# Kernel optimization log

Hardware: AMD Instinct MI355X
Metric: run time of the kernel (lower is better)

The kernel has to match this reference:

```python
import jax, jax.numpy as jnp
import numpy as np

N_NODES = 100000
N_EDGES = 1600000
D_IN = 128
D_OUT = 128


def setup_inputs() -> dict:
    key = jax.random.key(0)
    ks = jax.random.split(key, 7)
    x = jax.random.normal(ks[0], (N_NODES, D_IN), dtype=jnp.float32)
    edge_index = jax.random.randint(ks[1], (2, N_EDGES), 0, N_NODES, dtype=jnp.int64)
    edge_weights = jax.random.uniform(ks[2], (N_EDGES,), dtype=jnp.float32)
    s = 1.0 / np.sqrt(D_IN)
    W_lin = jax.random.uniform(ks[3], (D_IN, D_OUT), minval=-s, maxval=s, dtype=jnp.float32)
    b_lin = jax.random.uniform(ks[4], (D_OUT,), minval=-s, maxval=s, dtype=jnp.float32)
    W_agg = jax.random.uniform(ks[5], (D_IN, D_OUT), minval=-s, maxval=s, dtype=jnp.float32)
    b_agg = jax.random.uniform(ks[6], (D_OUT,), minval=-s, maxval=s, dtype=jnp.float32)
    return {"x": x, "edge_index": edge_index, "edge_weights": edge_weights,
            "W_lin": W_lin, "b_lin": b_lin, "W_agg": W_agg, "b_agg": b_agg}


def reference(x, edge_index, edge_weights, W_lin, b_lin, W_agg, b_agg):
    # self transform: [N, D_out]
    self_features = x @ W_lin + b_lin
    row, col = edge_index[0], edge_index[1]
    # gather neighbor features along edges: [E, D_in]
    neighbor_features = x[col] * edge_weights[:, None]
    # per-edge transform: [E, D_out]
    msgs = neighbor_features @ W_agg + b_agg
    # scatter-add to destination nodes (index_add_ on row)
    aggregated = jax.ops.segment_sum(msgs, row, num_segments=x.shape[0])
    return self_features + aggregated
```

## Files before the change

kernel.cpp:

```cpp
#include <hip/hip_runtime.h>

#define N_NODES 100000
#define N_EDGES 1600000
#define D 128
#define SCAN_CHUNK 1024
#define NB_SCAN ((N_NODES + SCAN_CHUNK - 1) / SCAN_CHUNK)

#define BSHIFT 9
#define BUCK_NODES 512
#define NBUCK 196
#define SCAP 10240
#define PART_CHUNK 4096
#define PART_BLOCKS ((N_EDGES + PART_CHUNK - 1) / PART_CHUNK)
#define CONV_BLOCKS 6250
#define W_BLOCKS 128
#define OCT_DIV 12500

typedef __attribute__((ext_vector_type(8))) short bf16x8;
typedef __attribute__((ext_vector_type(4))) float f32x4;
typedef __attribute__((ext_vector_type(4))) unsigned u32x4;

__device__ __forceinline__ unsigned bf16rne(float f) {
  unsigned u = __float_as_uint(f);
  return (u + 0x7fffu + ((u >> 16) & 1u)) >> 16;
}

#define T5_OFF    200
#define T5_FRAGW  100304
#define T5_SRT    116688
#define T5_XH     3316688
#define T5_ZH     9718736
#define WS_T5_BYTES ((size_t)16120784 * 4)

#define WS_OFF   100000
#define WS_BSUM  200004
#define WS_SRT   200192
#define WS_XH    3400192
#define WS_T1_BYTES ((size_t)3400192 * 4)
#define WS_T2_BYTES ((size_t)(3400192 + 6400000) * 4)

__global__ __launch_bounds__(256) void part_kernel(
    const int* __restrict__ ei, const float* __restrict__ ew,
    const float* __restrict__ x,
    const float* __restrict__ Wl, const float* __restrict__ Wa,
    int* __restrict__ pcur, int2* __restrict__ stage,
    uint4* __restrict__ xh4, unsigned short* __restrict__ fragW) {
  __shared__ int cntL[256];
  __shared__ int s0[256];
  __shared__ int gb[NBUCK];
  __shared__ int curL[NBUCK];
  __shared__ int2 recL[PART_CHUNK];
  __shared__ unsigned char buckL[PART_CHUNK];
  int bid = blockIdx.x, tid = threadIdx.x;

  if (bid < PART_BLOCKS) {
    cntL[tid] = 0;
    __syncthreads();
    int e0 = bid * PART_CHUNK;
    int tot = min(PART_CHUNK, N_EDGES - e0);
#pragma unroll
    for (int k = 0; k < PART_CHUNK / 256; k++) {
      int e = e0 + k * 256 + tid;
      if (e < N_EDGES) atomicAdd(&cntL[ei[e] >> BSHIFT], 1);
    }
    __syncthreads();
    for (int o = 1; o < 256; o <<= 1) {
      int add = (tid >= o) ? s0[tid - o] : 0;
      if (o == 1) add = (tid >= 1) ? cntL[tid - 1] : 0;
      if (o == 1) s0[tid] = cntL[tid];
      __syncthreads();
      if (o > 1) s0[tid] += add;
      else s0[tid] += add - cntL[tid] + cntL[tid];
      __syncthreads();
    }
    s0[tid] = cntL[tid];
    __syncthreads();
    for (int o = 1; o < 256; o <<= 1) {
      int add = (tid >= o) ? s0[tid - o] : 0;
      __syncthreads();
      s0[tid] += add;
      __syncthreads();
    }
    if (tid < NBUCK) {
      gb[tid] = atomicAdd(&pcur[tid], cntL[tid]);
      curL[tid] = 0;
    }
    __syncthreads();
#pragma unroll
    for (int k = 0; k < PART_CHUNK / 256; k++) {
      int e = e0 + k * 256 + tid;
      if (e < N_EDGES) {
        int d = ei[e];
        int src = ei[N_EDGES + e];
        float w = ew[e];
        int b = d >> BSHIFT;
        int r = atomicAdd(&curL[b], 1);
        int slot = (s0[b] - cntL[b]) + r;
        recL[slot] = make_int2(src | ((d & (BUCK_NODES - 1)) << 17),
                               __float_as_int(w));
        buckL[slot] = (unsigned char)b;
      }
    }
    __syncthreads();
    for (int i = tid; i < tot; i += 256) {
      int b = buckL[i];
      int idx = gb[b] + (i - (s0[b] - cntL[b]));
      stage[(size_t)b * SCAP + idx] = recL[i];
    }
  } else if (bid < PART_BLOCKS + CONV_BLOCKS) {
    int g = (bid - PART_BLOCKS) * 256 + tid;
    const u32x4* xp = reinterpret_cast<const u32x4*>(x);
    u32x4 a = __builtin_nontemporal_load(xp + (size_t)g * 2);
    u32x4 b = __builtin_nontemporal_load(xp + (size_t)g * 2 + 1);
    uint4 o;
    o.x = bf16rne(__uint_as_float(a.x)) | (bf16rne(__uint_as_float(a.y)) << 16);
    o.y = bf16rne(__uint_as_float(a.z)) | (bf16rne(__uint_as_float(a.w)) << 16);
    o.z = bf16rne(__uint_as_float(b.x)) | (bf16rne(__uint_as_float(b.y)) << 16);
    o.w = bf16rne(__uint_as_float(b.z)) | (bf16rne(__uint_as_float(b.w)) << 16);
    xh4[g] = o;
  } else {
    int tau = (bid - PART_BLOCKS - CONV_BLOCKS) * 256 + tid;
    int slot = tau >> 3, j = tau & 7;
    int lane = slot & 63, ft = slot >> 6;
    int t = ft & 7, s = ft >> 3;
    int kl = (s & 3) * 32 + (lane >> 4) * 8 + j;
    int n = t * 16 + (lane & 15);
    float v = (s < 4 ? Wl : Wa)[kl * 128 + n];
    fragW[slot * 8 + j] = (unsigned short)bf16rne(v);
  }
}

__global__ __launch_bounds__(512) void binB2_kernel(const int* __restrict__ pcur,
                                                    const int2* __restrict__ stage,
                                                    int* __restrict__ off,
                                                    int2* __restrict__ srt) {
  __shared__ int pc[NBUCK];
  __shared__ int h[BUCK_NODES * 8];
  __shared__ int sa[BUCK_NODES];
  __shared__ int cur8[BUCK_NODES * 8];
  __shared__ int baseS, mS;
  int b = blockIdx.x, tid = threadIdx.x;
  if (tid < NBUCK) pc[tid] = pcur[tid];
  for (int i = tid; i < BUCK_NODES * 8; i += 512) h[i] = 0;
  __syncthreads();
  if (tid == 0) {
    int s = 0;
    for (int i = 0; i < b; i++) s += pc[i];
    baseS = s;
    mS = pc[b];
  }
  __syncthreads();
  int base = baseS, m = mS;
  const int2* sp = stage + (size_t)b * SCAP;
  for (int r = tid; r < m; r += 512) {
    int rx = sp[r].x;
    int lsrc = rx & 0x1FFFF;
    int ldst = ((unsigned)rx) >> 17;
    atomicAdd(&h[(ldst << 3) + lsrc / OCT_DIV], 1);
  }
  __syncthreads();
  int tot = 0;
#pragma unroll
  for (int j = 0; j < 8; j++) tot += h[(tid << 3) + j];
  sa[tid] = tot;
  __syncthreads();
  for (int o = 1; o < BUCK_NODES; o <<= 1) {
    int add = (tid >= o) ? sa[tid - o] : 0;
    __syncthreads();
    sa[tid] += add;
    __syncthreads();
  }
  int nodeExcl = sa[tid] - tot;
  {
    int run = nodeExcl;
#pragma unroll
    for (int j = 0; j < 8; j++) {
      cur8[(tid << 3) + j] = run;
      run += h[(tid << 3) + j];
    }
  }
  int nb = b << BSHIFT;
  int nn = min(BUCK_NODES, N_NODES - nb);
  if (tid < nn) off[nb + tid] = base + nodeExcl;
  if (tid == 0 && b == NBUCK - 1) off[N_NODES] = base + m;
  __syncthreads();
  for (int r = tid; r < m; r += 512) {
    int2 rec = sp[r];
    int lsrc = rec.x & 0x1FFFF;
    int ldst = ((unsigned)rec.x) >> 17;
    int s = atomicAdd(&cur8[(ldst << 3) + lsrc / OCT_DIV], 1);
    srt[base + s] = make_int2(lsrc, rec.y);
  }
}

__global__ __launch_bounds__(256) void gather_zh_kernel(const unsigned* __restrict__ xh,
                                                        const int* __restrict__ off,
                                                        const int2* __restrict__ srt,
                                                        unsigned* __restrict__ zh) {
  int gid = blockIdx.x * 256 + threadIdx.x;
  int n = gid >> 5;
  int lane = gid & 31;
  int beg = off[n], end = off[n + 1];
  float4 acc = make_float4(0.f, 0.f, 0.f, 0.f);
  int e = beg;
  for (; e + 3 < end; e += 4) {
    int2 r0 = srt[e];
    int2 r1 = srt[e + 1];
    int2 r2 = srt[e + 2];
    int2 r3 = srt[e + 3];
    uint2 p0 = *reinterpret_cast<const uint2*>(xh + (size_t)r0.x * 64 + lane * 2);
    uint2 p1 = *reinterpret_cast<const uint2*>(xh + (size_t)r1.x * 64 + lane * 2);
    uint2 p2 = *reinterpret_cast<const uint2*>(xh + (size_t)r2.x * 64 + lane * 2);
    uint2 p3 = *reinterpret_cast<const uint2*>(xh + (size_t)r3.x * 64 + lane * 2);
    float w0 = __int_as_float(r0.y), w1 = __int_as_float(r1.y);
    float w2 = __int_as_float(r2.y), w3 = __int_as_float(r3.y);
    acc.x = fmaf(w0, __uint_as_float(p0.x << 16), acc.x);
    acc.y = fmaf(w0, __uint_as_float(p0.x & 0xffff0000u), acc.y);
    acc.z = fmaf(w0, __uint_as_float(p0.y << 16), acc.z);
    acc.w = fmaf(w0, __uint_as_float(p0.y & 0xffff0000u), acc.w);
    acc.x = fmaf(w1, __uint_as_float(p1.x << 16), acc.x);
    acc.y = fmaf(w1, __uint_as_float(p1.x & 0xffff0000u), acc.y);
    acc.z = fmaf(w1, __uint_as_float(p1.y << 16), acc.z);
    acc.w = fmaf(w1, __uint_as_float(p1.y & 0xffff0000u), acc.w);
    acc.x = fmaf(w2, __uint_as_float(p2.x << 16), acc.x);
    acc.y = fmaf(w2, __uint_as_float(p2.x & 0xffff0000u), acc.y);
    acc.z = fmaf(w2, __uint_as_float(p2.y << 16), acc.z);
    acc.w = fmaf(w2, __uint_as_float(p2.y & 0xffff0000u), acc.w);
    acc.x = fmaf(w3, __uint_as_float(p3.x << 16), acc.x);
    acc.y = fmaf(w3, __uint_as_float(p3.x & 0xffff0000u), acc.y);
    acc.z = fmaf(w3, __uint_as_float(p3.y << 16), acc.z);
    acc.w = fmaf(w3, __uint_as_float(p3.y & 0xffff0000u), acc.w);
  }
  for (; e < end; e++) {
    int2 r0 = srt[e];
    uint2 p0 = *reinterpret_cast<const uint2*>(xh + (size_t)r0.x * 64 + lane * 2);
    float w0 = __int_as_float(r0.y);
    acc.x = fmaf(w0, __uint_as_float(p0.x << 16), acc.x);
    acc.y = fmaf(w0, __uint_as_float(p0.x & 0xffff0000u), acc.y);
    acc.z = fmaf(w0, __uint_as_float(p0.y << 16), acc.z);
    acc.w = fmaf(w0, __uint_as_float(p0.y & 0xffff0000u), acc.w);
  }
  uint2 o;
  o.x = bf16rne(acc.x) | (bf16rne(acc.y) << 16);
  o.y = bf16rne(acc.z) | (bf16rne(acc.w) << 16);
  *reinterpret_cast<uint2*>(zh + (size_t)n * 64 + lane * 2) = o;
}

__global__ __launch_bounds__(256) void mfma_gemm_kernel(
    const short* __restrict__ xh, const short* __restrict__ zh,
    const short* __restrict__ fragW, const int* __restrict__ off,
    const float* __restrict__ bl, const float* __restrict__ ba,
    float* __restrict__ out) {
  int tid = threadIdx.x;
  int wave = tid >> 6, lane = tid & 63;
  int m = lane & 15, q = lane >> 4;
  int R = blockIdx.x * 64 + wave * 16;
  const short* xrow = xh + (size_t)(R + m) * D + q * 8;
  const short* zrow = zh + (size_t)(R + m) * D + q * 8;
  const short* fw = fragW + (size_t)lane * 8;

  f32x4 acc[8];
#pragma unroll
  for (int t = 0; t < 8; t++) acc[t] = (f32x4){0.f, 0.f, 0.f, 0.f};

#pragma unroll
  for (int s = 0; s < 8; s++) {
    bf16x8 a = *reinterpret_cast<const bf16x8*>(s < 4 ? xrow + s * 32
                                                      : zrow + (s - 4) * 32);
#pragma unroll
    for (int t = 0; t < 8; t++) {
      bf16x8 b = *reinterpret_cast<const bf16x8*>(fw + (size_t)((s * 8 + t) * 64) * 8);
      acc[t] = __builtin_amdgcn_mfma_f32_16x16x32_bf16(a, b, acc[t], 0, 0, 0);
    }
  }

  float blv[8], bav[8];
#pragma unroll
  for (int t = 0; t < 8; t++) {
    blv[t] = bl[t * 16 + m];
    bav[t] = ba[t * 16 + m];
  }
#pragma unroll
  for (int r = 0; r < 4; r++) {
    int row = R + q * 4 + r;
    if (row < N_NODES) {
      float dg = (float)(off[row + 1] - off[row]);
#pragma unroll
      for (int t = 0; t < 8; t++)
        __builtin_nontemporal_store(acc[t][r] + blv[t] + dg * bav[t],
                                    out + (size_t)row * D + t * 16 + m);
    }
  }
}


__global__ __launch_bounds__(256) void hist_kernel(const int* __restrict__ ei,
                                                   int* __restrict__ cnt) {
  int e = blockIdx.x * 256 + threadIdx.x;
  if (e < N_EDGES) atomicAdd(&cnt[ei[e]], 1);
}

__global__ __launch_bounds__(256) void block_sum_kernel(const int* __restrict__ cnt,
                                                        int* __restrict__ bsum) {
  int base = blockIdx.x * SCAN_CHUNK;
  int s = 0;
#pragma unroll
  for (int k = 0; k < 4; k++) {
    int i = base + (int)threadIdx.x + k * 256;
    if (i < N_NODES) s += cnt[i];
  }
  __shared__ int red[4];
  for (int o = 32; o > 0; o >>= 1) s += __shfl_down(s, o, 64);
  if ((threadIdx.x & 63) == 0) red[threadIdx.x >> 6] = s;
  __syncthreads();
  if (threadIdx.x == 0) bsum[blockIdx.x] = red[0] + red[1] + red[2] + red[3];
}

__global__ __launch_bounds__(128) void scan_bsum_kernel(int* __restrict__ bsum,
                                                        int* __restrict__ off) {
  __shared__ int sh[128];
  int t = threadIdx.x;
  int v = (t < NB_SCAN) ? bsum[t] : 0;
  sh[t] = v;
  __syncthreads();
  for (int o = 1; o < 128; o <<= 1) {
    int add = (t >= o) ? sh[t - o] : 0;
    __syncthreads();
    sh[t] += add;
    __syncthreads();
  }
  if (t < NB_SCAN) bsum[t] = sh[t] - v;
  if (t == 0) off[N_NODES] = sh[127];
}

__global__ __launch_bounds__(256) void scan_offsets_kernel(const int* __restrict__ cnt,
                                                           const int* __restrict__ bsum,
                                                           int* __restrict__ off) {
  __shared__ int sh[256];
  int t = threadIdx.x;
  int i0 = blockIdx.x * SCAN_CHUNK + t * 4;
  int c[4];
#pragma unroll
  for (int k = 0; k < 4; k++) c[k] = (i0 + k < N_NODES) ? cnt[i0 + k] : 0;
  int ls = c[0] + c[1] + c[2] + c[3];
  sh[t] = ls;
  __syncthreads();
  for (int o = 1; o < 256; o <<= 1) {
    int add = (t >= o) ? sh[t - o] : 0;
    __syncthreads();
    sh[t] += add;
    __syncthreads();
  }
  int run = bsum[blockIdx.x] + sh[t] - ls;
#pragma unroll
  for (int k = 0; k < 4; k++) {
    if (i0 + k < N_NODES) off[i0 + k] = run;
    run += c[k];
  }
}

__global__ __launch_bounds__(256) void fill_kernel(const int* __restrict__ ei,
                                                   const float* __restrict__ ew,
                                                   const int* __restrict__ off,
                                                   int* __restrict__ cur,
                                                   int2* __restrict__ srt) {
  int e = blockIdx.x * 256 + threadIdx.x;
  if (e >= N_EDGES) return;
  int dst = ei[e];
  int p = off[dst] + atomicAdd(&cur[dst], 1);
  srt[p] = make_int2(ei[N_EDGES + e], __float_as_int(ew[e]));
}

__global__ __launch_bounds__(256) void convert_kernel(const float* __restrict__ x,
                                                      uint4* __restrict__ xh) {
  int i = blockIdx.x * 256 + threadIdx.x;
  const float4* xp = reinterpret_cast<const float4*>(x);
  float4 a = xp[(size_t)i * 2];
  float4 b = xp[(size_t)i * 2 + 1];
  uint4 o;
  o.x = bf16rne(a.x) | (bf16rne(a.y) << 16);
  o.y = bf16rne(a.z) | (bf16rne(a.w) << 16);
  o.z = bf16rne(b.x) | (bf16rne(b.y) << 16);
  o.w = bf16rne(b.z) | (bf16rne(b.w) << 16);
  xh[i] = o;
}

__global__ __launch_bounds__(256) void gather_bf16_kernel(const unsigned* __restrict__ xh,
                                                          const int* __restrict__ off,
                                                          const int2* __restrict__ srt,
                                                          float* __restrict__ z,
                                                          float* __restrict__ degf) {
  int gid = blockIdx.x * 256 + threadIdx.x;
  int n = gid >> 5;
  int lane = gid & 31;
  if (n >= N_NODES) return;
  int beg = off[n], end = off[n + 1];
  float4 acc = make_float4(0.f, 0.f, 0.f, 0.f);
  int e = beg;
  for (; e + 1 < end; e += 2) {
    int2 r0 = srt[e];
    int2 r1 = srt[e + 1];
    uint2 p0 = *reinterpret_cast<const uint2*>(xh + (size_t)r0.x * 64 + lane * 2);
    uint2 p1 = *reinterpret_cast<const uint2*>(xh + (size_t)r1.x * 64 + lane * 2);
    float w0 = __int_as_float(r0.y);
    float w1 = __int_as_float(r1.y);
    acc.x = fmaf(w0, __uint_as_float(p0.x << 16), acc.x);
    acc.y = fmaf(w0, __uint_as_float(p0.x & 0xffff0000u), acc.y);
    acc.z = fmaf(w0, __uint_as_float(p0.y << 16), acc.z);
    acc.w = fmaf(w0, __uint_as_float(p0.y & 0xffff0000u), acc.w);
    acc.x = fmaf(w1, __uint_as_float(p1.x << 16), acc.x);
    acc.y = fmaf(w1, __uint_as_float(p1.x & 0xffff0000u), acc.y);
    acc.z = fmaf(w1, __uint_as_float(p1.y << 16), acc.z);
    acc.w = fmaf(w1, __uint_as_float(p1.y & 0xffff0000u), acc.w);
  }
  if (e < end) {
    int2 r0 = srt[e];
    uint2 p0 = *reinterpret_cast<const uint2*>(xh + (size_t)r0.x * 64 + lane * 2);
    float w0 = __int_as_float(r0.y);
    acc.x = fmaf(w0, __uint_as_float(p0.x << 16), acc.x);
    acc.y = fmaf(w0, __uint_as_float(p0.x & 0xffff0000u), acc.y);
    acc.z = fmaf(w0, __uint_as_float(p0.y << 16), acc.z);
    acc.w = fmaf(w0, __uint_as_float(p0.y & 0xffff0000u), acc.w);
  }
  *reinterpret_cast<float4*>(z + (size_t)n * D + (lane << 2)) = acc;
  if (lane == 0) degf[n] = (float)(end - beg);
}

__global__ __launch_bounds__(256) void gather_f32_kernel(const float* __restrict__ x,
                                                         const int* __restrict__ off,
                                                         const int2* __restrict__ srt,
                                                         float* __restrict__ z,
                                                         float* __restrict__ degf) {
  int gid = blockIdx.x * 256 + threadIdx.x;
  int n = gid >> 5;
  int lane = gid & 31;
  if (n >= N_NODES) return;
  int beg = off[n], end = off[n + 1];
  float4 acc = make_float4(0.f, 0.f, 0.f, 0.f);
  for (int e = beg; e < end; e++) {
    int2 r0 = srt[e];
    float4 x0 = *reinterpret_cast<const float4*>(x + (size_t)r0.x * D + (lane << 2));
    float w0 = __int_as_float(r0.y);
    acc.x = fmaf(w0, x0.x, acc.x); acc.y = fmaf(w0, x0.y, acc.y);
    acc.z = fmaf(w0, x0.z, acc.z); acc.w = fmaf(w0, x0.w, acc.w);
  }
  *reinterpret_cast<float4*>(z + (size_t)n * D + (lane << 2)) = acc;
  if (lane == 0) degf[n] = (float)(end - beg);
}

__global__ __launch_bounds__(256) void scatter_kernel(const float* __restrict__ x,
                                                      const int* __restrict__ ei,
                                                      const float* __restrict__ ew,
                                                      float* __restrict__ z,
                                                      float* __restrict__ deg) {
  long long g = (long long)blockIdx.x * 256 + threadIdx.x;
  int e = (int)(g >> 5);
  int lane = (int)(g & 31);
  if (e >= N_EDGES) return;
  int dst = ei[e];
  int src = ei[N_EDGES + e];
  float w = ew[e];
  float4 xv = *reinterpret_cast<const float4*>(x + (size_t)src * D + (lane << 2));
  float* o = z + (size_t)dst * D + (lane << 2);
  atomicAdd(o + 0, w * xv.x);
  atomicAdd(o + 1, w * xv.y);
  atomicAdd(o + 2, w * xv.z);
  atomicAdd(o + 3, w * xv.w);
  if (lane == 0) atomicAdd(deg + dst, 1.0f);
}

__global__ __launch_bounds__(256) void fused_gemm_kernel(const float* __restrict__ x,
                                                         const float* __restrict__ Wl,
                                                         const float* __restrict__ bl,
                                                         const float* __restrict__ Wa,
                                                         const float* __restrict__ ba,
                                                         const float* __restrict__ deg,
                                                         float* __restrict__ out) {
  __shared__ float xs[32 * 16];
  __shared__ float zs[32 * 16];
  __shared__ float wls[16 * 128];
  __shared__ float was[16 * 128];
  const int tid = threadIdx.x;
  const int row0 = blockIdx.x * 32;
  const int c4 = tid & 31;
  const int r0 = tid >> 5;
  float4 acc[4];
#pragma unroll
  for (int i = 0; i < 4; i++) acc[i] = make_float4(0.f, 0.f, 0.f, 0.f);

  for (int k0 = 0; k0 < D; k0 += 16) {
    {
      int t = tid & 127;
      int r = t >> 2;
      int kc = (t & 3) << 2;
      const float* sp = (tid < 128) ? x : out;
      float* dp = (tid < 128) ? xs : zs;
      *reinterpret_cast<float4*>(dp + r * 16 + kc) =
          *reinterpret_cast<const float4*>(sp + (size_t)(row0 + r) * D + k0 + kc);
    }
#pragma unroll
    for (int i = 0; i < 2; i++) {
      int f = tid + i * 256;
      int kk = f >> 5;
      int cc = (f & 31) << 2;
      *reinterpret_cast<float4*>(wls + kk * 128 + cc) =
          *reinterpret_cast<const float4*>(Wl + (size_t)(k0 + kk) * D + cc);
      *reinterpret_cast<float4*>(was + kk * 128 + cc) =
          *reinterpret_cast<const float4*>(Wa + (size_t)(k0 + kk) * D + cc);
    }
    __syncthreads();
#pragma unroll
    for (int kk = 0; kk < 16; kk++) {
      float4 wl = *reinterpret_cast<const float4*>(wls + kk * 128 + (c4 << 2));
      float4 wa = *reinterpret_cast<const float4*>(was + kk * 128 + (c4 << 2));
#pragma unroll
      for (int rr = 0; rr < 4; rr++) {
        int r2 = r0 + rr * 8;
        float xv = xs[r2 * 16 + kk];
        float zv = zs[r2 * 16 + kk];
        acc[rr].x = fmaf(xv, wl.x, fmaf(zv, wa.x, acc[rr].x));
        acc[rr].y = fmaf(xv, wl.y, fmaf(zv, wa.y, acc[rr].y));
        acc[rr].z = fmaf(xv, wl.z, fmaf(zv, wa.z, acc[rr].z));
        acc[rr].w = fmaf(xv, wl.w, fmaf(zv, wa.w, acc[rr].w));
      }
    }
    __syncthreads();
  }

  float4 blv = *reinterpret_cast<const float4*>(bl + (c4 << 2));
  float4 bav = *reinterpret_cast<const float4*>(ba + (c4 << 2));
#pragma unroll
  for (int rr = 0; rr < 4; rr++) {
    int r = row0 + r0 + rr * 8;
    float d = deg[r];
    float4 o;
    o.x = acc[rr].x + blv.x + d * bav.x;
    o.y = acc[rr].y + blv.y + d * bav.y;
    o.z = acc[rr].z + blv.z + d * bav.z;
    o.w = acc[rr].w + blv.w + d * bav.w;
    *reinterpret_cast<float4*>(out + (size_t)r * D + (c4 << 2)) = o;
  }
}

extern "C" void kernel_launch(void* const* d_in, const int* in_sizes, int n_in,
                              void* d_out, int out_size, void* d_ws, size_t ws_size,
                              hipStream_t stream) {
  const float* x  = (const float*)d_in[0];
  const int*   ei = (const int*)d_in[1];
  const float* ew = (const float*)d_in[2];
  const float* Wl = (const float*)d_in[3];
  const float* bl = (const float*)d_in[4];
  const float* Wa = (const float*)d_in[5];
  const float* ba = (const float*)d_in[6];
  float* out = (float*)d_out;

  if (ws_size >= WS_T5_BYTES) {
    int* pcur = (int*)d_ws;
    int* off = pcur + T5_OFF;
    unsigned short* fragW = (unsigned short*)(pcur + T5_FRAGW);
    int2* srt = (int2*)(pcur + T5_SRT);
    unsigned* xh = (unsigned*)(pcur + T5_XH);
    unsigned* zh = (unsigned*)(pcur + T5_ZH);
    int2* stage = (int2*)(pcur + T5_ZH);

    hipMemsetAsync(pcur, 0, NBUCK * sizeof(int), stream);
    part_kernel<<<PART_BLOCKS + CONV_BLOCKS + W_BLOCKS, 256, 0, stream>>>(
        ei, ew, x, Wl, Wa, pcur, stage, (uint4*)xh, fragW);
    binB2_kernel<<<NBUCK, 512, 0, stream>>>(pcur, stage, off, srt);
    gather_zh_kernel<<<N_NODES * 32 / 256, 256, 0, stream>>>(xh, off, srt, zh);
    mfma_gemm_kernel<<<1563, 256, 0, stream>>>((const short*)xh, (const short*)zh,
                                               (const short*)fragW, off, bl, ba, out);
  } else if (ws_size >= WS_T1_BYTES) {
    int*  cnt  = (int*)d_ws;
    int*  off  = cnt + WS_OFF;
    int*  bsum = cnt + WS_BSUM;
    int2* srt  = (int2*)(cnt + WS_SRT);
    float* degf = (float*)cnt;

    hipMemsetAsync(cnt, 0, (size_t)N_NODES * sizeof(int), stream);
    hist_kernel<<<(N_EDGES + 255) / 256, 256, 0, stream>>>(ei, cnt);
    block_sum_kernel<<<NB_SCAN, 256, 0, stream>>>(cnt, bsum);
    scan_bsum_kernel<<<1, 128, 0, stream>>>(bsum, off);
    scan_offsets_kernel<<<NB_SCAN, 256, 0, stream>>>(cnt, bsum, off);
    hipMemsetAsync(cnt, 0, (size_t)N_NODES * sizeof(int), stream);
    fill_kernel<<<(N_EDGES + 255) / 256, 256, 0, stream>>>(ei, ew, off, cnt, srt);

    if (ws_size >= WS_T2_BYTES) {
      unsigned* xh = (unsigned*)(cnt + WS_XH);
      convert_kernel<<<(N_NODES * D / 8) / 256, 256, 0, stream>>>(x, (uint4*)xh);
      gather_bf16_kernel<<<(N_NODES * 32 + 255) / 256, 256, 0, stream>>>(xh, off, srt, out, degf);
    } else {
      gather_f32_kernel<<<(N_NODES * 32 + 255) / 256, 256, 0, stream>>>(x, off, srt, out, degf);
    }
    fused_gemm_kernel<<<N_NODES / 32, 256, 0, stream>>>(x, Wl, bl, Wa, ba, degf, out);
  } else {
    float* deg = (float*)d_ws;
    hipMemsetAsync(out, 0, (size_t)N_NODES * D * sizeof(float), stream);
    hipMemsetAsync(deg, 0, (size_t)N_NODES * sizeof(float), stream);
    scatter_kernel<<<(N_EDGES * 32) / 256, 256, 0, stream>>>(x, ei, ew, out, deg);
    fused_gemm_kernel<<<N_NODES / 32, 256, 0, stream>>>(x, Wl, bl, Wa, ba, deg, out);
  }
}
```

Before: 271.3 us.

## Fuse neighbor gather into MFMA GEMM and simplify per-node binning

Removes the separate gather kernel that wrote the aggregated neighbor features (zh) to global memory. The MFMA GEMM kernel now gathers and weights neighbor rows itself, packs the sums to bf16 in registers and feeds them straight in as the A operand, which saves a global round trip of an N×128 bf16 tensor and one launch. The binning kernel drops the source-octant sub-bucketing (8x histogram) in favor of a plain per-destination count and a double-buffered scan, and a redundant scan in the partition kernel is deleted. The cost is that each GEMM lane now walks its own node's edge list, so the gather has lower parallelism (one lane row per node across 16 rows per wave) and uneven degrees cause divergence. Dropping the source-sorted order may also reduce cache locality of the gathers.

After: 263.7 us. -2.8%, faster.

```diff
diff --git a/kernel.cpp b/kernel.cpp
--- a/kernel.cpp
+++ b/kernel.cpp
@@ -14,7 +14,6 @@
 #define PART_BLOCKS ((N_EDGES + PART_CHUNK - 1) / PART_CHUNK)
 #define CONV_BLOCKS 6250
 #define W_BLOCKS 128
-#define OCT_DIV 12500
 
 typedef __attribute__((ext_vector_type(8))) short bf16x8;
 typedef __attribute__((ext_vector_type(4))) float f32x4;
@@ -64,15 +63,6 @@
       if (e < N_EDGES) atomicAdd(&cntL[ei[e] >> BSHIFT], 1);
     }
     __syncthreads();
-    for (int o = 1; o < 256; o <<= 1) {
-      int add = (tid >= o) ? s0[tid - o] : 0;
-      if (o == 1) add = (tid >= 1) ? cntL[tid - 1] : 0;
-      if (o == 1) s0[tid] = cntL[tid];
-      __syncthreads();
-      if (o > 1) s0[tid] += add;
-      else s0[tid] += add - cntL[tid] + cntL[tid];
-      __syncthreads();
-    }
     s0[tid] = cntL[tid];
     __syncthreads();
     for (int o = 1; o < 256; o <<= 1) {
@@ -135,13 +125,13 @@
                                                     int* __restrict__ off,
                                                     int2* __restrict__ srt) {
   __shared__ int pc[NBUCK];
-  __shared__ int h[BUCK_NODES * 8];
   __shared__ int sa[BUCK_NODES];
-  __shared__ int cur8[BUCK_NODES * 8];
+  __shared__ int sb[BUCK_NODES];
+  __shared__ int curL[BUCK_NODES];
   __shared__ int baseS, mS;
   int b = blockIdx.x, tid = threadIdx.x;
   if (tid < NBUCK) pc[tid] = pcur[tid];
-  for (int i = tid; i < BUCK_NODES * 8; i += 512) h[i] = 0;
+  if (tid < BUCK_NODES) sa[tid] = 0;
   __syncthreads();
   if (tid == 0) {
     int s = 0;
@@ -152,121 +142,118 @@
   __syncthreads();
   int base = baseS, m = mS;
   const int2* sp = stage + (size_t)b * SCAP;
-  for (int r = tid; r < m; r += 512) {
-    int rx = sp[r].x;
-    int lsrc = rx & 0x1FFFF;
-    int ldst = ((unsigned)rx) >> 17;
-    atomicAdd(&h[(ldst << 3) + lsrc / OCT_DIV], 1);
-  }
-  __syncthreads();
-  int tot = 0;
-#pragma unroll
-  for (int j = 0; j < 8; j++) tot += h[(tid << 3) + j];
-  sa[tid] = tot;
-  __syncthreads();
+  for (int r = tid; r < m; r += 512)
+    atomicAdd(&sa[((unsigned)sp[r].x) >> 17], 1);
+  __syncthreads();
+  int* srcb = sa;
+  int* dstb = sb;
   for (int o = 1; o < BUCK_NODES; o <<= 1) {
-    int add = (tid >= o) ? sa[tid - o] : 0;
-    __syncthreads();
-    sa[tid] += add;
-    __syncthreads();
-  }
-  int nodeExcl = sa[tid] - tot;
-  {
-    int run = nodeExcl;
-#pragma unroll
-    for (int j = 0; j < 8; j++) {
-      cur8[(tid << 3) + j] = run;
-      run += h[(tid << 3) + j];
-    }
+    if (tid < BUCK_NODES)
+      dstb[tid] = srcb[tid] + (tid >= o ? srcb[tid - o] : 0);
+    __syncthreads();
+    int* t = srcb; srcb = dstb; dstb = t;
   }
   int nb = b << BSHIFT;
   int nn = min(BUCK_NODES, N_NODES - nb);
-  if (tid < nn) off[nb + tid] = base + nodeExcl;
-  if (tid == 0 && b == NBUCK - 1) off[N_NODES] = base + m;
+  if (tid < BUCK_NODES) {
+    int ex = tid ? srcb[tid - 1] : 0;
+    curL[tid] = ex;
+    if (tid < nn) off[nb + tid] = base + ex;
+  }
+  if (tid == 0 && b == NBUCK - 1) off[N_NODES] = base + srcb[nn - 1];
   __syncthreads();
   for (int r = tid; r < m; r += 512) {
     int2 rec = sp[r];
-    int lsrc = rec.x & 0x1FFFF;
     int ldst = ((unsigned)rec.x) >> 17;
-    int s = atomicAdd(&cur8[(ldst << 3) + lsrc / OCT_DIV], 1);
-    srt[base + s] = make_int2(lsrc, rec.y);
-  }
-}
-
-__global__ __launch_bounds__(256) void gather_zh_kernel(const unsigned* __restrict__ xh,
-                                                        const int* __restrict__ off,
-                                                        const int2* __restrict__ srt,
-                                                        unsigned* __restrict__ zh) {
-  int gid = blockIdx.x * 256 + threadIdx.x;
-  int n = gid >> 5;
-  int lane = gid & 31;
-  int beg = off[n], end = off[n + 1];
-  float4 acc = make_float4(0.f, 0.f, 0.f, 0.f);
-  int e = beg;
-  for (; e + 3 < end; e += 4) {
-    int2 r0 = srt[e];
-    int2 r1 = srt[e + 1];
-    int2 r2 = srt[e + 2];
-    int2 r3 = srt[e + 3];
-    uint2 p0 = *reinterpret_cast<const uint2*>(xh + (size_t)r0.x * 64 + lane * 2);
-    uint2 p1 = *reinterpret_cast<const uint2*>(xh + (size_t)r1.x * 64 + lane * 2);
-    uint2 p2 = *reinterpret_cast<const uint2*>(xh + (size_t)r2.x * 64 + lane * 2);
-    uint2 p3 = *reinterpret_cast<const uint2*>(xh + (size_t)r3.x * 64 + lane * 2);
-    float w0 = __int_as_float(r0.y), w1 = __int_as_float(r1.y);
-    float w2 = __int_as_float(r2.y), w3 = __int_as_float(r3.y);
-    acc.x = fmaf(w0, __uint_as_float(p0.x << 16), acc.x);
-    acc.y = fmaf(w0, __uint_as_float(p0.x & 0xffff0000u), acc.y);
-    acc.z = fmaf(w0, __uint_as_float(p0.y << 16), acc.z);
-    acc.w = fmaf(w0, __uint_as_float(p0.y & 0xffff0000u), acc.w);
-    acc.x = fmaf(w1, __uint_as_float(p1.x << 16), acc.x);
-    acc.y = fmaf(w1, __uint_as_float(p1.x & 0xffff0000u), acc.y);
-    acc.z = fmaf(w1, __uint_as_float(p1.y << 16), acc.z);
-    acc.w = fmaf(w1, __uint_as_float(p1.y & 0xffff0000u), acc.w);
-    acc.x = fmaf(w2, __uint_as_float(p2.x << 16), acc.x);
-    acc.y = fmaf(w2, __uint_as_float(p2.x & 0xffff0000u), acc.y);
-    acc.z = fmaf(w2, __uint_as_float(p2.y << 16), acc.z);
-    acc.w = fmaf(w2, __uint_as_float(p2.y & 0xffff0000u), acc.w);
-    acc.x = fmaf(w3, __uint_as_float(p3.x << 16), acc.x);
-    acc.y = fmaf(w3, __uint_as_float(p3.x & 0xffff0000u), acc.y);
-    acc.z = fmaf(w3, __uint_as_float(p3.y << 16), acc.z);
-    acc.w = fmaf(w3, __uint_as_float(p3.y & 0xffff0000u), acc.w);
-  }
-  for (; e < end; e++) {
-    int2 r0 = srt[e];
-    uint2 p0 = *reinterpret_cast<const uint2*>(xh + (size_t)r0.x * 64 + lane * 2);
-    float w0 = __int_as_float(r0.y);
-    acc.x = fmaf(w0, __uint_as_float(p0.x << 16), acc.x);
-    acc.y = fmaf(w0, __uint_as_float(p0.x & 0xffff0000u), acc.y);
-    acc.z = fmaf(w0, __uint_as_float(p0.y << 16), acc.z);
-    acc.w = fmaf(w0, __uint_as_float(p0.y & 0xffff0000u), acc.w);
-  }
-  uint2 o;
-  o.x = bf16rne(acc.x) | (bf16rne(acc.y) << 16);
-  o.y = bf16rne(acc.z) | (bf16rne(acc.w) << 16);
-  *reinterpret_cast<uint2*>(zh + (size_t)n * 64 + lane * 2) = o;
-}
-
-__global__ __launch_bounds__(256) void mfma_gemm_kernel(
-    const short* __restrict__ xh, const short* __restrict__ zh,
+    int s = atomicAdd(&curL[ldst], 1);
+    srt[base + s] = make_int2(rec.x & 0x1FFFF, rec.y);
+  }
+}
+
+#define FACC(s_, p_, w_)                                                    \
+  {                                                                         \
+    acc1[s_][0] = fmaf(w_, __uint_as_float((p_).x << 16), acc1[s_][0]);     \
+    acc1[s_][1] = fmaf(w_, __uint_as_float((p_).x & 0xffff0000u), acc1[s_][1]); \
+    acc1[s_][2] = fmaf(w_, __uint_as_float((p_).y << 16), acc1[s_][2]);     \
+    acc1[s_][3] = fmaf(w_, __uint_as_float((p_).y & 0xffff0000u), acc1[s_][3]); \
+    acc1[s_][4] = fmaf(w_, __uint_as_float((p_).z << 16), acc1[s_][4]);     \
+    acc1[s_][5] = fmaf(w_, __uint_as_float((p_).z & 0xffff0000u), acc1[s_][5]); \
+    acc1[s_][6] = fmaf(w_, __uint_as_float((p_).w << 16), acc1[s_][6]);     \
+    acc1[s_][7] = fmaf(w_, __uint_as_float((p_).w & 0xffff0000u), acc1[s_][7]); \
+  }
+
+__global__ __launch_bounds__(256) void fused_gather_gemm_kernel(
+    const uint4* __restrict__ xh4, const short* __restrict__ xh,
     const short* __restrict__ fragW, const int* __restrict__ off,
+    const int2* __restrict__ srt,
     const float* __restrict__ bl, const float* __restrict__ ba,
     float* __restrict__ out) {
   int tid = threadIdx.x;
   int wave = tid >> 6, lane = tid & 63;
   int m = lane & 15, q = lane >> 4;
   int R = blockIdx.x * 64 + wave * 16;
-  const short* xrow = xh + (size_t)(R + m) * D + q * 8;
-  const short* zrow = zh + (size_t)(R + m) * D + q * 8;
+  int n = R + m;
+
+  float acc1[4][8];
+#pragma unroll
+  for (int s = 0; s < 4; s++)
+#pragma unroll
+    for (int j = 0; j < 8; j++) acc1[s][j] = 0.f;
+
+  int beg = 0, end = 0;
+  if (n < N_NODES) {
+    beg = off[n];
+    end = off[n + 1];
+  }
+  int e = beg;
+  for (; e + 1 < end; e += 2) {
+    int2 r0 = srt[e];
+    int2 r1 = srt[e + 1];
+    uint4 p00 = xh4[(size_t)r0.x * 16 + 0 * 4 + q];
+    uint4 p01 = xh4[(size_t)r0.x * 16 + 1 * 4 + q];
+    uint4 p02 = xh4[(size_t)r0.x * 16 + 2 * 4 + q];
+    uint4 p03 = xh4[(size_t)r0.x * 16 + 3 * 4 + q];
+    uint4 p10 = xh4[(size_t)r1.x * 16 + 0 * 4 + q];
+    uint4 p11 = xh4[(size_t)r1.x * 16 + 1 * 4 + q];
+    uint4 p12 = xh4[(size_t)r1.x * 16 + 2 * 4 + q];
+    uint4 p13 = xh4[(size_t)r1.x * 16 + 3 * 4 + q];
+    float w0 = __int_as_float(r0.y), w1 = __int_as_float(r1.y);
+    FACC(0, p00, w0) FACC(1, p01, w0) FACC(2, p02, w0) FACC(3, p03, w0)
+    FACC(0, p10, w1) FACC(1, p11, w1) FACC(2, p12, w1) FACC(3, p13, w1)
+  }
+  if (e < end) {
+    int2 r0 = srt[e];
+    uint4 p00 = xh4[(size_t)r0.x * 16 + 0 * 4 + q];
+    uint4 p01 = xh4[(size_t)r0.x * 16 + 1 * 4 + q];
+    uint4 p02 = xh4[(size_t)r0.x * 16 + 2 * 4 + q];
+    uint4 p03 = xh4[(size_t)r0.x * 16 + 3 * 4 + q];
+    float w0 = __int_as_float(r0.y);
+    FACC(0, p00, w0) FACC(1, p01, w0) FACC(2, p02, w0) FACC(3, p03, w0)
+  }
+
+  bf16x8 az[4];
+#pragma unroll
+  for (int s = 0; s < 4; s++) {
+    union { bf16x8 v; unsigned u[4]; } cv;
+#pragma unroll
+    for (int jj = 0; jj < 4; jj++)
+      cv.u[jj] = bf16rne(acc1[s][2 * jj]) | (bf16rne(acc1[s][2 * jj + 1]) << 16);
+    az[s] = cv.v;
+  }
+
+  const short* xrow = xh + (size_t)n * D + q * 8;
   const short* fw = fragW + (size_t)lane * 8;
-
   f32x4 acc[8];
 #pragma unroll
   for (int t = 0; t < 8; t++) acc[t] = (f32x4){0.f, 0.f, 0.f, 0.f};
 
 #pragma unroll
   for (int s = 0; s < 8; s++) {
-    bf16x8 a = *reinterpret_cast<const bf16x8*>(s < 4 ? xrow + s * 32
-                                                      : zrow + (s - 4) * 32);
+    bf16x8 a;
+    if (s < 4)
+      a = *reinterpret_cast<const bf16x8*>(xrow + s * 32);
+    else
+      a = az[s - 4];
 #pragma unroll
     for (int t = 0; t < 8; t++) {
       bf16x8 b = *reinterpret_cast<const bf16x8*>(fw + (size_t)((s * 8 + t) * 64) * 8);
@@ -560,16 +547,15 @@
     unsigned short* fragW = (unsigned short*)(pcur + T5_FRAGW);
     int2* srt = (int2*)(pcur + T5_SRT);
     unsigned* xh = (unsigned*)(pcur + T5_XH);
-    unsigned* zh = (unsigned*)(pcur + T5_ZH);
     int2* stage = (int2*)(pcur + T5_ZH);
 
     hipMemsetAsync(pcur, 0, NBUCK * sizeof(int), stream);
     part_kernel<<<PART_BLOCKS + CONV_BLOCKS + W_BLOCKS, 256, 0, stream>>>(
         ei, ew, x, Wl, Wa, pcur, stage, (uint4*)xh, fragW);
     binB2_kernel<<<NBUCK, 512, 0, stream>>>(pcur, stage, off, srt);
-    gather_zh_kernel<<<N_NODES * 32 / 256, 256, 0, stream>>>(xh, off, srt, zh);
-    mfma_gemm_kernel<<<1563, 256, 0, stream>>>((const short*)xh, (const short*)zh,
-                                               (const short*)fragW, off, bl, ba, out);
+    fused_gather_gemm_kernel<<<1563, 256, 0, stream>>>(
+        (const uint4*)xh, (const short*)xh, (const short*)fragW, off, srt,
+        bl, ba, out);
   } else if (ws_size >= WS_T1_BYTES) {
     int*  cnt  = (int*)d_ws;
     int*  off  = cnt + WS_OFF;
```
